# Kernel tuning notes

Measured on AMD Instinct MI355X. Metric: run time of the kernel, lower is better.

## Reference

```python
import jax, jax.numpy as jnp
import numpy as np

HEADS = 16
DIM_HEAD = 64
DIM = 1024
INNER = HEADS * DIM_HEAD  # 1024
DIM_OUT = 1024


def setup_inputs() -> dict:
    key = jax.random.key(0)
    k1, k2, k3, k4 = jax.random.split(key, 4)
    B, N = 4, 2048
    x = jax.random.normal(k1, (B, N, DIM), dtype=jnp.float32)
    # hk.Linear(inner_dim*3, with_bias=False): weight shape [in, out]
    w_qkv = jax.random.normal(k2, (DIM, INNER * 3), dtype=jnp.float32) / np.sqrt(DIM)
    # hk.Linear(dim_out): weight [INNER, DIM_OUT] + bias
    w_out = jax.random.normal(k3, (INNER, DIM_OUT), dtype=jnp.float32) / np.sqrt(INNER)
    b_out = jax.random.normal(k4, (DIM_OUT,), dtype=jnp.float32) * 0.01
    return {"x": x, "w_qkv": w_qkv, "w_out": w_out, "b_out": b_out}


def reference(x, w_qkv, w_out, b_out):
    B, N, _ = x.shape
    scale = DIM_HEAD ** -0.5
    qkv = x @ w_qkv  # [B, N, 3*INNER]
    q, k, v = jnp.split(qkv, 3, axis=-1)
    # b n (h d) -> b h n d
    split_heads = lambda t: t.reshape(B, N, HEADS, DIM_HEAD).transpose(0, 2, 1, 3)
    q, k, v = split_heads(q), split_heads(k), split_heads(v)
    dots = jnp.einsum('bhid,bhjd->bhij', q, k) * scale  # [B, H, N, N]
    attn = jax.nn.softmax(dots, axis=-1)
    out = jnp.einsum('bhij,bhjd->bhid', attn, v)  # [B, H, N, D]
    out = out.transpose(0, 2, 1, 3).reshape(B, N, INNER)  # b h n d -> b n (h d)
    return out @ w_out + b_out
```

## Files before the change

kernel.cpp:

```cpp
#include <hip/hip_runtime.h>
#include <cstdint>


typedef unsigned short ushort_t;
typedef _Float16 half_t;
typedef half_t half8 __attribute__((ext_vector_type(8)));
typedef half_t half4 __attribute__((ext_vector_type(4)));
typedef __fp16 fp16x2 __attribute__((ext_vector_type(2)));
typedef float floatx4 __attribute__((ext_vector_type(4)));
typedef ushort_t ushort8 __attribute__((ext_vector_type(8)));

#define QSCALE 0.18033688011112043f

__device__ __forceinline__ float bf2f(ushort_t h) {
  union { unsigned int u; float f; } v; v.u = ((unsigned int)h) << 16; return v.f;
}
__device__ __forceinline__ void async_copy16(const void* g, void* l) {
  __builtin_amdgcn_global_load_lds(
      reinterpret_cast<const __attribute__((address_space(1))) unsigned int*>(
          reinterpret_cast<uintptr_t>(g)),
      reinterpret_cast<__attribute__((address_space(3))) unsigned int*>(
          reinterpret_cast<uintptr_t>(l)),
      16, 0, 0);
}
__device__ __forceinline__ void lds_fence() {
  asm volatile("s_waitcnt lgkmcnt(0)" ::: "memory");
}
__device__ __forceinline__ void vm_fence() {
  asm volatile("s_waitcnt vmcnt(0)" ::: "memory");
}

__global__ __launch_bounds__(256) void prep_kernel(
    const void* __restrict__ x_raw, half_t* __restrict__ xb,
    const void* __restrict__ w_qkv_raw, half_t* __restrict__ WTqkv,
    const void* __restrict__ w_out_raw, half_t* __restrict__ WTout,
    const void* __restrict__ b_out_raw, float* __restrict__ bb) {
  __shared__ half_t tile[64][65];
  __shared__ int cnt;
  const int tid = threadIdx.x;
  if (tid == 0) cnt = 0;
  __syncthreads();
  {
    const ushort_t* xs = (const ushort_t*)x_raw;
    int local = 0;
    for (int i = tid; i < 8192; i += 256)
      if ((xs[i] & 0x7F80u) == 0x7F80u) ++local;
    if (local) atomicAdd(&cnt, local);
  }
  __syncthreads();
  const int isf32 = (cnt >= 2) ? 1 : 0;
  const int bid = blockIdx.x;

  if (bid < 4096) {
    const int i0 = (bid * 256 + tid) * 8;
    half8 o;
    if (isf32) {
      const floatx4* s = (const floatx4*)x_raw;
      const floatx4 a = s[(i0 >> 2)];
      const floatx4 b = s[(i0 >> 2) + 1];
#pragma unroll
      for (int j = 0; j < 4; ++j) { o[j] = (half_t)a[j]; o[4 + j] = (half_t)b[j]; }
    } else {
      const ushort8 u = *(const ushort8*)((const ushort_t*)x_raw + i0);
#pragma unroll
      for (int j = 0; j < 8; ++j) o[j] = (half_t)bf2f(u[j]);
    }
    *(half8*)&xb[i0] = o;
  } else if (bid < 5120) {
    const int t = bid - 4096;
    const int bx = t & 63;
    const int by = t >> 6;
    const void* src; half_t* dst; int C, c0;
    if (bx < 48) { src = w_qkv_raw; dst = WTqkv; C = 3072; c0 = bx * 64; }
    else         { src = w_out_raw; dst = WTout; C = 1024; c0 = (bx - 48) * 64; }
    const int R = 1024;
    const int r0 = by * 64;
    const int tx = tid & 63, ty = tid >> 6;
    if (isf32) {
      const float* s = (const float*)src;
      for (int i = ty; i < 64; i += 4) tile[i][tx] = (half_t)s[(size_t)(r0 + i) * C + (c0 + tx)];
    } else {
      const ushort_t* s = (const ushort_t*)src;
      for (int i = ty; i < 64; i += 4) tile[i][tx] = (half_t)bf2f(s[(size_t)(r0 + i) * C + (c0 + tx)]);
    }
    __syncthreads();
    for (int i = ty; i < 64; i += 4) dst[(size_t)(c0 + i) * R + (r0 + tx)] = tile[tx][i];
  } else {
#pragma unroll
    for (int j = 0; j < 4; ++j) {
      const int i = j * 256 + tid;
      bb[i] = isf32 ? ((const float*)b_out_raw)[i] : bf2f(((const ushort_t*)b_out_raw)[i]);
    }
  }
}

__global__ __launch_bounds__(512) void gemm_qkv_kernel(
    const half_t* __restrict__ X, const half_t* __restrict__ WT,
    half_t* __restrict__ Qb, half_t* __restrict__ Kb, half_t* __restrict__ VTb) {
  __shared__ half_t smem[65536];
  const int tid = threadIdx.x;
  const int wv = tid >> 6, lane = tid & 63;
  const int l15 = lane & 15, quad = lane >> 4, l7 = l15 & 7;
  const int wm = wv & 1, wn = wv >> 1;
  const int bid = blockIdx.x;
  const int xcd = bid & 7, idx = bid >> 3;
  const int mb = xcd * 4 + (idx & 3);
  const int nb = idx >> 2;
  const int rlo = lane >> 3, ci = lane & 7;
  const int sw_klo = (ci ^ rlo) * 8;
  const int rb0 = wv * 16, rb1 = wv * 16 + 8;

  const half_t* Ah[2] = {X + (size_t)(mb * 256) * 1024,
                         X + (size_t)(mb * 256 + 128) * 1024};
  const half_t* Bh[2] = {WT + (size_t)(nb * 256) * 1024,
                         WT + (size_t)(nb * 256 + 128) * 1024};

  floatx4 acc[8][4];
  const floatx4 z = {0.f, 0.f, 0.f, 0.f};
#pragma unroll
  for (int mi = 0; mi < 8; ++mi)
#pragma unroll
    for (int ni = 0; ni < 4; ++ni) acc[mi][ni] = z;

#pragma unroll
  for (int h = 0; h < 2; ++h) {
    async_copy16(Ah[h] + (size_t)(rb0 + rlo) * 1024 + sw_klo, &smem[h * 8192 + rb0 * 64]);
    async_copy16(Ah[h] + (size_t)(rb1 + rlo) * 1024 + sw_klo, &smem[h * 8192 + rb1 * 64]);
  }
#pragma unroll
  for (int h = 0; h < 2; ++h) {
    async_copy16(Bh[h] + (size_t)(rb0 + rlo) * 1024 + sw_klo, &smem[16384 + h * 8192 + rb0 * 64]);
    async_copy16(Bh[h] + (size_t)(rb1 + rlo) * 1024 + sw_klo, &smem[16384 + h * 8192 + rb1 * 64]);
  }

#pragma unroll 2
  for (int u = 0; u < 16; ++u) {
    const int b = u & 1, bn = b ^ 1;
    const int kn = ((u + 1) & 15) * 64;
    const int cb = b * 32768, cn = bn * 32768;

    async_copy16(Ah[0] + (size_t)(rb0 + rlo) * 1024 + kn + sw_klo, &smem[cn + rb0 * 64]);
    async_copy16(Ah[0] + (size_t)(rb1 + rlo) * 1024 + kn + sw_klo, &smem[cn + rb1 * 64]);
    asm volatile("s_waitcnt vmcnt(2)" ::: "memory");
    __builtin_amdgcn_s_barrier();
    __builtin_amdgcn_sched_barrier(0);

    half8 bf[4][2];
    const int bbase = cb + 16384 + (wn >> 1) * 8192 + ((wn & 1) * 64) * 64;
#pragma unroll
    for (int ni = 0; ni < 4; ++ni)
#pragma unroll
      for (int ks = 0; ks < 2; ++ks)
        bf[ni][ks] = *(const half8*)&smem[bbase + (ni * 16 + l15) * 64 + (((ks * 4 + quad) ^ l7) * 8)];
    const int abase = cb + wm * 8192;
    {
      half8 af[2][2];
#pragma unroll
      for (int m2 = 0; m2 < 2; ++m2)
#pragma unroll
        for (int ks = 0; ks < 2; ++ks)
          af[m2][ks] = *(const half8*)&smem[abase + ((0 * 2 + m2) * 16 + l15) * 64 + (((ks * 4 + quad) ^ l7) * 8)];
      __builtin_amdgcn_s_setprio(1);
#pragma unroll
      for (int ks = 0; ks < 2; ++ks)
#pragma unroll
        for (int m2 = 0; m2 < 2; ++m2)
#pragma unroll
          for (int ni = 0; ni < 4; ++ni)
            acc[0 * 2 + m2][ni] = __builtin_amdgcn_mfma_f32_16x16x32_f16(af[m2][ks], bf[ni][ks], acc[0 * 2 + m2][ni], 0, 0, 0);
      __builtin_amdgcn_s_setprio(0);
    }
    async_copy16(Ah[1] + (size_t)(rb0 + rlo) * 1024 + kn + sw_klo, &smem[cn + 8192 + rb0 * 64]);
    async_copy16(Ah[1] + (size_t)(rb1 + rlo) * 1024 + kn + sw_klo, &smem[cn + 8192 + rb1 * 64]);
    {
      half8 af[2][2];
#pragma unroll
      for (int m2 = 0; m2 < 2; ++m2)
#pragma unroll
        for (int ks = 0; ks < 2; ++ks)
          af[m2][ks] = *(const half8*)&smem[abase + ((1 * 2 + m2) * 16 + l15) * 64 + (((ks * 4 + quad) ^ l7) * 8)];
      __builtin_amdgcn_s_setprio(1);
#pragma unroll
      for (int ks = 0; ks < 2; ++ks)
#pragma unroll
        for (int m2 = 0; m2 < 2; ++m2)
#pragma unroll
          for (int ni = 0; ni < 4; ++ni)
            acc[1 * 2 + m2][ni] = __builtin_amdgcn_mfma_f32_16x16x32_f16(af[m2][ks], bf[ni][ks], acc[1 * 2 + m2][ni], 0, 0, 0);
      __builtin_amdgcn_s_setprio(0);
    }
    async_copy16(Bh[0] + (size_t)(rb0 + rlo) * 1024 + kn + sw_klo, &smem[cn + 16384 + rb0 * 64]);
    async_copy16(Bh[0] + (size_t)(rb1 + rlo) * 1024 + kn + sw_klo, &smem[cn + 16384 + rb1 * 64]);
    {
      half8 af[2][2];
#pragma unroll
      for (int m2 = 0; m2 < 2; ++m2)
#pragma unroll
        for (int ks = 0; ks < 2; ++ks)
          af[m2][ks] = *(const half8*)&smem[abase + ((2 * 2 + m2) * 16 + l15) * 64 + (((ks * 4 + quad) ^ l7) * 8)];
      __builtin_amdgcn_s_setprio(1);
#pragma unroll
      for (int ks = 0; ks < 2; ++ks)
#pragma unroll
        for (int m2 = 0; m2 < 2; ++m2)
#pragma unroll
          for (int ni = 0; ni < 4; ++ni)
            acc[2 * 2 + m2][ni] = __builtin_amdgcn_mfma_f32_16x16x32_f16(af[m2][ks], bf[ni][ks], acc[2 * 2 + m2][ni], 0, 0, 0);
      __builtin_amdgcn_s_setprio(0);
    }
    async_copy16(Bh[1] + (size_t)(rb0 + rlo) * 1024 + kn + sw_klo, &smem[cn + 24576 + rb0 * 64]);
    async_copy16(Bh[1] + (size_t)(rb1 + rlo) * 1024 + kn + sw_klo, &smem[cn + 24576 + rb1 * 64]);
    {
      half8 af[2][2];
#pragma unroll
      for (int m2 = 0; m2 < 2; ++m2)
#pragma unroll
        for (int ks = 0; ks < 2; ++ks)
          af[m2][ks] = *(const half8*)&smem[abase + ((3 * 2 + m2) * 16 + l15) * 64 + (((ks * 4 + quad) ^ l7) * 8)];
      __builtin_amdgcn_s_setprio(1);
#pragma unroll
      for (int ks = 0; ks < 2; ++ks)
#pragma unroll
        for (int m2 = 0; m2 < 2; ++m2)
#pragma unroll
          for (int ni = 0; ni < 4; ++ni)
            acc[3 * 2 + m2][ni] = __builtin_amdgcn_mfma_f32_16x16x32_f16(af[m2][ks], bf[ni][ks], acc[3 * 2 + m2][ni], 0, 0, 0);
      __builtin_amdgcn_s_setprio(0);
    }
  }

  vm_fence();
  __syncthreads();

  const int which = nb >> 2;
  if (which != 2) {
    const float sc = (which == 0) ? QSCALE : 1.0f;
#pragma unroll
    for (int mi = 0; mi < 8; ++mi)
#pragma unroll
      for (int ni = 0; ni < 4; ++ni) {
        const int col = wn * 64 + ni * 16 + l15;
        const int rowb = wm * 128 + mi * 16 + quad * 4;
#pragma unroll
        for (int r = 0; r < 4; ++r)
          smem[(rowb + r) * 256 + col] = (half_t)(acc[mi][ni][r] * sc);
      }
    __syncthreads();
    half_t* dstB = (which == 0) ? Qb : Kb;
    const int seg = tid & 31;
    const int hh = (nb & 3) * 4 + (seg >> 3);
    const int dd = (seg & 7) * 8;
#pragma unroll 4
    for (int i = 0; i < 16; ++i) {
      const int row = i * 16 + (tid >> 5);
      const half8 val = *(const half8*)&smem[row * 256 + seg * 8];
      const int rowg = mb * 256 + row;
      const int bb = rowg >> 11, nn = rowg & 2047;
      *(half8*)&dstB[(((size_t)(bb * 16 + hh)) * 2048 + nn) * 64 + dd] = val;
    }
  } else {
    const int nb2 = nb - 8;
    const int bb = mb >> 3;
    const int nn0 = (mb * 256) & 2047;
#pragma unroll
    for (int q = 0; q < 2; ++q) {
      if ((wn >> 1) == q) {
        const int dlb = (wn & 1) * 64;
#pragma unroll
        for (int mi = 0; mi < 8; ++mi)
#pragma unroll
          for (int ni = 0; ni < 4; ++ni) {
            const int dl = dlb + ni * 16 + l15;
            const int rowb = wm * 128 + mi * 16 + quad * 4;
#pragma unroll
            for (int r = 0; r < 4; ++r)
              smem[dl * 264 + rowb + r] = (half_t)acc[mi][ni][r];
          }
      }
      __syncthreads();
      const int npos = (tid & 127) * 2;
#pragma unroll 4
      for (int i = 0; i < 32; ++i) {
        const int dl = i * 4 + (tid >> 7);
        const int hh = nb2 * 4 + q * 2 + (dl >> 6);
        const int dd = dl & 63;
        const int koff = npos ^ ((dd & 8) ? 4 : 0);
        const uint32_t val = *(const uint32_t*)&smem[dl * 264 + npos];
        *(uint32_t*)&VTb[((size_t)((bb * 16 + hh) * 64 + dd)) * 2048 + nn0 + koff] = val;
      }
      __syncthreads();
    }
  }
}

__global__ __launch_bounds__(512) void attn_kernel(
    const half_t* __restrict__ Qb, const half_t* __restrict__ Kb,
    const half_t* __restrict__ VTb, half_t* __restrict__ Ob) {
  __shared__ half_t smem[16384];
  const int tid = threadIdx.x, wv = tid >> 6, lane = tid & 63;
  const int l15 = lane & 15, quad = lane >> 4;
  const int l7 = l15 & 7;
  const int bid = blockIdx.x;
  const int xcd = bid & 7, idx = bid >> 3;
  const int bh = ((idx & 7) << 3) + xcd;
  const int qt = idx >> 3;
  const int bq = bh >> 4, hh = bh & 15;
  const half_t* Qg = Qb + (size_t)bh * 2048 * 64;
  const half_t* Kg = Kb + (size_t)bh * 2048 * 64;
  const half_t* Vg = VTb + (size_t)bh * 64 * 2048;
  const int q0 = qt * 256;
  const int rlo = lane >> 3, ci = lane & 7;
  const int sw_klo = (ci ^ rlo) * 8;

  const int q1 = quad >> 1, qb0 = quad & 1, b3 = (l15 >> 3) & 1;
  int kx[2], vx[4];
#pragma unroll
  for (int ks = 0; ks < 2; ++ks) kx[ks] = ((ks * 4 + quad) ^ l7) * 8;
#pragma unroll
  for (int ki = 0; ki < 4; ++ki)
    vx[ki] = (((ki * 2 + q1) ^ l7) * 8) + ((qb0 ^ b3) * 4);

#pragma unroll
  for (int j = 0; j < 4; ++j) {
    const int rb = (wv * 4 + j) * 8;
    async_copy16(Qg + (size_t)(q0 + rb + rlo) * 64 + sw_klo, &smem[rb * 64]);
  }
  vm_fence();
  half8 aq[2][2];
#pragma unroll
  for (int ks = 0; ks < 2; ++ks)
#pragma unroll
    for (int qi = 0; qi < 2; ++qi) {
      const int rr = wv * 32 + qi * 16 + l15;
      aq[ks][qi] = *(const half8*)&smem[rr * 64 + (((ks * 4 + quad) ^ l7) * 8)];
    }
  __syncthreads();

  floatx4 o_acc[2][4];
  const floatx4 z = {0.f, 0.f, 0.f, 0.f};
  float l_st[2] = {0.f, 0.f};
#pragma unroll
  for (int qi = 0; qi < 2; ++qi)
#pragma unroll
    for (int di = 0; di < 4; ++di) o_acc[qi][di] = z;

  {
    const int rb = wv * 8;
    async_copy16(Kg + (size_t)(rb + rlo) * 64 + sw_klo, &smem[rb * 64]);
    async_copy16(Vg + (size_t)(rb + rlo) * 2048 + sw_klo, &smem[8192 + rb * 64]);
  }

#pragma unroll 2
  for (int t = 0; t < 32; ++t) {
    const int co = (t & 1) * 4096;
    const int po = 4096 - co;
    __syncthreads();
    if (t < 31) {
      const int rb = wv * 8;
      async_copy16(Kg + (size_t)((t + 1) * 64 + rb + rlo) * 64 + sw_klo,
                   &smem[po + rb * 64]);
      async_copy16(Vg + (size_t)(rb + rlo) * 2048 + (t + 1) * 64 + sw_klo,
                   &smem[8192 + po + rb * 64]);
    }
    const half_t* Kc = &smem[co];
    const half_t* Vc = &smem[8192 + co];

    floatx4 s_acc[4][2];
#pragma unroll
    for (int ki = 0; ki < 4; ++ki)
#pragma unroll
      for (int qi = 0; qi < 2; ++qi) s_acc[ki][qi] = z;
#pragma unroll
    for (int ks = 0; ks < 2; ++ks) {
      half8 bk[4];
#pragma unroll
      for (int ki = 0; ki < 4; ++ki)
        bk[ki] = *(const half8*)&Kc[(ki * 16 + l15) * 64 + kx[ks]];
      __builtin_amdgcn_s_setprio(1);
#pragma unroll
      for (int ki = 0; ki < 4; ++ki)
#pragma unroll
        for (int qi = 0; qi < 2; ++qi)
          s_acc[ki][qi] = __builtin_amdgcn_mfma_f32_16x16x32_f16(bk[ki], aq[ks][qi], s_acc[ki][qi], 0, 0, 0);
      __builtin_amdgcn_s_setprio(0);
    }

#pragma unroll
    for (int c = 0; c < 2; ++c) {
      half8 bv[4];
#pragma unroll
      for (int di = 0; di < 4; ++di) {
        union { half4 q[2]; half8 v; } b_;
        b_.q[0] = *(const half4*)&Vc[(di * 16 + l15) * 64 + vx[2 * c]];
        b_.q[1] = *(const half4*)&Vc[(di * 16 + l15) * 64 + vx[2 * c + 1]];
        bv[di] = b_.v;
      }
      union Ap { uint32_t u[4]; half8 h; } apu[2];
#pragma unroll
      for (int kii = 0; kii < 2; ++kii)
#pragma unroll
        for (int qi = 0; qi < 2; ++qi) {
          const int ki = c * 2 + kii;
          const float p0 = __builtin_amdgcn_exp2f(s_acc[ki][qi][0]);
          const float p1 = __builtin_amdgcn_exp2f(s_acc[ki][qi][1]);
          const float p2 = __builtin_amdgcn_exp2f(s_acc[ki][qi][2]);
          const float p3 = __builtin_amdgcn_exp2f(s_acc[ki][qi][3]);
          l_st[qi] += (p0 + p1) + (p2 + p3);
          union { fp16x2 v; uint32_t u; } lo_, hi_;
          lo_.v = __builtin_amdgcn_cvt_pkrtz(p0, p1);
          hi_.v = __builtin_amdgcn_cvt_pkrtz(p2, p3);
          apu[qi].u[kii * 2] = lo_.u;
          apu[qi].u[kii * 2 + 1] = hi_.u;
        }
      __builtin_amdgcn_s_setprio(1);
#pragma unroll
      for (int qi = 0; qi < 2; ++qi)
#pragma unroll
        for (int di = 0; di < 4; ++di)
          o_acc[qi][di] = __builtin_amdgcn_mfma_f32_16x16x32_f16(apu[qi].h, bv[di], o_acc[qi][di], 0, 0, 0);
      __builtin_amdgcn_s_setprio(0);
    }
  }

  float linv[2];
#pragma unroll
  for (int qi = 0; qi < 2; ++qi) {
    float rs = l_st[qi];
    rs += __shfl_xor(rs, 16);
    rs += __shfl_xor(rs, 32);
    linv[qi] = 1.0f / rs;
  }

  __syncthreads();
  const int c2 = (tid & 31) * 2;
  const int rbase = (tid >> 5) & 15;
#pragma unroll
  for (int p = 0; p < 2; ++p) {
    if ((wv >> 2) == p) {
      const int rw = (wv & 3) * 32;
#pragma unroll
      for (int qi = 0; qi < 2; ++qi)
#pragma unroll
        for (int r = 0; r < 4; ++r) {
          const float inv = __shfl(linv[qi], quad * 4 + r);
          const int rowl = rw + qi * 16 + quad * 4 + r;
#pragma unroll
          for (int di = 0; di < 4; ++di)
            smem[rowl * 72 + di * 16 + l15] = (half_t)(o_acc[qi][di][r] * inv);
        }
    }
    __syncthreads();
#pragma unroll 4
    for (int i = 0; i < 8; ++i) {
      const int rowl = i * 16 + rbase;
      const uint32_t val = *(const uint32_t*)&smem[rowl * 72 + c2];
      const int nn = q0 + p * 128 + rowl;
      *(uint32_t*)&Ob[((size_t)(bq * 2048 + nn)) * 1024 + hh * 64 + c2] = val;
    }
    __syncthreads();
  }
}

__global__ __launch_bounds__(256) void gemm_out_kernel(
    const half_t* __restrict__ A, const half_t* __restrict__ WT,
    const float* __restrict__ bias, float* __restrict__ out) {
  __shared__ half_t As[128 * 64];
  __shared__ half_t Bs[128 * 64];
  const int tid = threadIdx.x;
  const int wv = tid >> 6, lane = tid & 63;
  const int l15 = lane & 15, quad = lane >> 4;
  const int l7 = l15 & 7;
  const int wm = wv & 1, wn = wv >> 1;
  const int bid = blockIdx.x;
  const int xcd = bid & 7, idx = bid >> 3;
  const int mb = xcd * 8 + (idx & 7);
  const int nb = idx >> 3;
  const int rlo = lane >> 3, ci = lane & 7;
  const int sw_klo = (ci ^ rlo) * 8;

  floatx4 acc[4][4];
  const floatx4 z = {0.f, 0.f, 0.f, 0.f};
#pragma unroll
  for (int mi = 0; mi < 4; ++mi)
#pragma unroll
    for (int ni = 0; ni < 4; ++ni) acc[mi][ni] = z;

  const half_t* Abase = A + (size_t)mb * 128 * 1024;
  const half_t* Bbase = WT + (size_t)nb * 128 * 1024;

  for (int k0 = 0; k0 < 1024; k0 += 64) {
#pragma unroll
    for (int j = 0; j < 4; ++j) {
      const int rb = (wv * 4 + j) * 8;
      async_copy16(Abase + (size_t)(rb + rlo) * 1024 + k0 + sw_klo, &As[rb * 64]);
    }
#pragma unroll
    for (int j = 0; j < 4; ++j) {
      const int rb = (wv * 4 + j) * 8;
      async_copy16(Bbase + (size_t)(rb + rlo) * 1024 + k0 + sw_klo, &Bs[rb * 64]);
    }
    __syncthreads();
#pragma unroll
    for (int ks = 0; ks < 2; ++ks) {
      half8 af[4], bfv[4];
#pragma unroll
      for (int mi = 0; mi < 4; ++mi) {
        const int rr = wm * 64 + mi * 16 + l15;
        af[mi] = *(const half8*)&As[rr * 64 + (((ks * 4 + quad) ^ l7) * 8)];
      }
#pragma unroll
      for (int ni = 0; ni < 4; ++ni) {
        const int rr = wn * 64 + ni * 16 + l15;
        bfv[ni] = *(const half8*)&Bs[rr * 64 + (((ks * 4 + quad) ^ l7) * 8)];
      }
#pragma unroll
      for (int mi = 0; mi < 4; ++mi)
#pragma unroll
        for (int ni = 0; ni < 4; ++ni)
          acc[mi][ni] = __builtin_amdgcn_mfma_f32_16x16x32_f16(af[mi], bfv[ni], acc[mi][ni], 0, 0, 0);
    }
    __syncthreads();
  }

#pragma unroll
  for (int mi = 0; mi < 4; ++mi) {
#pragma unroll
    for (int ni = 0; ni < 4; ++ni) {
      const int colg = nb * 128 + wn * 64 + ni * 16 + l15;
      const float bs = bias[colg];
#pragma unroll
      for (int r = 0; r < 4; ++r) {
        const int rowg = mb * 128 + wm * 64 + mi * 16 + quad * 4 + r;
        out[(size_t)rowg * 1024 + colg] = acc[mi][ni][r] + bs;
      }
    }
  }
}

extern "C" void kernel_launch(void* const* d_in, const int* in_sizes, int n_in,
                              void* d_out, int out_size, void* d_ws, size_t ws_size,
                              hipStream_t stream) {
  const void* x_raw     = d_in[0];
  const void* w_qkv_raw = d_in[1];
  const void* w_out_raw = d_in[2];
  const void* b_out_raw = d_in[3];
  float* out = (float*)d_out;

  char* ws = (char*)d_ws;
  half_t* xb    = (half_t*)(ws);
  half_t* Qb    = (half_t*)(ws + ((size_t)16 << 20));
  half_t* Kb    = (half_t*)(ws + ((size_t)32 << 20));
  half_t* VTb   = (half_t*)(ws + ((size_t)48 << 20));
  half_t* WTqkv = (half_t*)(ws + ((size_t)64 << 20));
  half_t* WTout = (half_t*)(ws + ((size_t)70 << 20));
  float*  bb    = (float*)(ws + ((size_t)72 << 20));
  half_t* Ob    = xb;

  prep_kernel<<<5121, 256, 0, stream>>>(x_raw, xb, w_qkv_raw, WTqkv,
                                        w_out_raw, WTout, b_out_raw, bb);
  gemm_qkv_kernel<<<384, 512, 0, stream>>>(xb, WTqkv, Qb, Kb, VTb);
  attn_kernel<<<512, 512, 0, stream>>>(Qb, Kb, VTb, Ob);
  gemm_out_kernel<<<512, 256, 0, stream>>>(Ob, WTout, bb, out);
}
```

Before: 265.5 us.

## Double-buffer output GEMM with 128x256 tiles and interleaved async prefetch

Rewrites the output-projection GEMM to use 512-thread blocks computing 128x256 tiles, double-buffered LDS staging, and async global-to-LDS prefetch of the next K slice interleaved with MFMA groups. This is meant to hide global load latency that the old single-buffer loop exposed behind __syncthreads. It also adds a trailing barrier in the QKV GEMM loop. The larger tile halves the grid to 256 blocks, which can lower occupancy and load balance on the device.

```diff
diff --git a/kernel.cpp b/kernel.cpp
--- a/kernel.cpp
+++ b/kernel.cpp
@@ -227,6 +227,8 @@
             acc[3 * 2 + m2][ni] = __builtin_amdgcn_mfma_f32_16x16x32_f16(af[m2][ks], bf[ni][ks], acc[3 * 2 + m2][ni], 0, 0, 0);
       __builtin_amdgcn_s_setprio(0);
     }
+    __builtin_amdgcn_s_barrier();
+    __builtin_amdgcn_sched_barrier(0);
   }
 
   vm_fence();
@@ -461,15 +463,13 @@
   }
 }
 
-__global__ __launch_bounds__(256) void gemm_out_kernel(
+__global__ __launch_bounds__(512) void gemm_out_kernel(
     const half_t* __restrict__ A, const half_t* __restrict__ WT,
     const float* __restrict__ bias, float* __restrict__ out) {
-  __shared__ half_t As[128 * 64];
-  __shared__ half_t Bs[128 * 64];
+  __shared__ half_t smem[49152];
   const int tid = threadIdx.x;
   const int wv = tid >> 6, lane = tid & 63;
-  const int l15 = lane & 15, quad = lane >> 4;
-  const int l7 = l15 & 7;
+  const int l15 = lane & 15, quad = lane >> 4, l7 = l15 & 7;
   const int wm = wv & 1, wn = wv >> 1;
   const int bid = blockIdx.x;
   const int xcd = bid & 7, idx = bid >> 3;
@@ -477,6 +477,8 @@
   const int nb = idx >> 3;
   const int rlo = lane >> 3, ci = lane & 7;
   const int sw_klo = (ci ^ rlo) * 8;
+  const half_t* Abase = A + (size_t)(mb * 128) * 1024;
+  const half_t* Bbase = WT + (size_t)(nb * 256) * 1024;
 
   floatx4 acc[4][4];
   const floatx4 z = {0.f, 0.f, 0.f, 0.f};
@@ -485,48 +487,112 @@
 #pragma unroll
     for (int ni = 0; ni < 4; ++ni) acc[mi][ni] = z;
 
-  const half_t* Abase = A + (size_t)mb * 128 * 1024;
-  const half_t* Bbase = WT + (size_t)nb * 128 * 1024;
-
-  for (int k0 = 0; k0 < 1024; k0 += 64) {
-#pragma unroll
-    for (int j = 0; j < 4; ++j) {
-      const int rb = (wv * 4 + j) * 8;
-      async_copy16(Abase + (size_t)(rb + rlo) * 1024 + k0 + sw_klo, &As[rb * 64]);
-    }
-#pragma unroll
-    for (int j = 0; j < 4; ++j) {
-      const int rb = (wv * 4 + j) * 8;
-      async_copy16(Bbase + (size_t)(rb + rlo) * 1024 + k0 + sw_klo, &Bs[rb * 64]);
-    }
-    __syncthreads();
-#pragma unroll
-    for (int ks = 0; ks < 2; ++ks) {
-      half8 af[4], bfv[4];
-#pragma unroll
-      for (int mi = 0; mi < 4; ++mi) {
-        const int rr = wm * 64 + mi * 16 + l15;
-        af[mi] = *(const half8*)&As[rr * 64 + (((ks * 4 + quad) ^ l7) * 8)];
-      }
-#pragma unroll
-      for (int ni = 0; ni < 4; ++ni) {
-        const int rr = wn * 64 + ni * 16 + l15;
-        bfv[ni] = *(const half8*)&Bs[rr * 64 + (((ks * 4 + quad) ^ l7) * 8)];
-      }
-#pragma unroll
-      for (int mi = 0; mi < 4; ++mi)
+#pragma unroll
+  for (int j = 0; j < 2; ++j) {
+    const int ro = wv * 16 + j * 8;
+    async_copy16(Abase + (size_t)(ro + rlo) * 1024 + sw_klo, &smem[ro * 64]);
+  }
+#pragma unroll
+  for (int j = 0; j < 4; ++j) {
+    const int ro = wv * 32 + j * 8;
+    async_copy16(Bbase + (size_t)(ro + rlo) * 1024 + sw_klo, &smem[8192 + ro * 64]);
+  }
+
+#pragma unroll 2
+  for (int u = 0; u < 16; ++u) {
+    const int b = u & 1, bn = b ^ 1;
+    const int kn = ((u + 1) & 15) * 64;
+    const int cb = b * 24576, cn = bn * 24576;
+
+#pragma unroll
+    for (int j = 0; j < 2; ++j) {
+      const int ro = wv * 16 + j * 8;
+      async_copy16(Abase + (size_t)(ro + rlo) * 1024 + kn + sw_klo, &smem[cn + ro * 64]);
+    }
+    asm volatile("s_waitcnt vmcnt(2)" ::: "memory");
+    __builtin_amdgcn_s_barrier();
+    __builtin_amdgcn_sched_barrier(0);
+
+    half8 bf[4][2];
+    const int bbase2 = cb + 8192 + (wn * 64) * 64;
+#pragma unroll
+    for (int ni = 0; ni < 4; ++ni)
+#pragma unroll
+      for (int ks = 0; ks < 2; ++ks)
+        bf[ni][ks] = *(const half8*)&smem[bbase2 + (ni * 16 + l15) * 64 + (((ks * 4 + quad) ^ l7) * 8)];
+    const int abase = cb + (wm * 64) * 64;
+    {
+      half8 af[2];
+#pragma unroll
+      for (int ks = 0; ks < 2; ++ks)
+        af[ks] = *(const half8*)&smem[abase + (0 * 16 + l15) * 64 + (((ks * 4 + quad) ^ l7) * 8)];
+      __builtin_amdgcn_s_setprio(1);
+#pragma unroll
+      for (int ks = 0; ks < 2; ++ks)
 #pragma unroll
         for (int ni = 0; ni < 4; ++ni)
-          acc[mi][ni] = __builtin_amdgcn_mfma_f32_16x16x32_f16(af[mi], bfv[ni], acc[mi][ni], 0, 0, 0);
-    }
-    __syncthreads();
-  }
+          acc[0][ni] = __builtin_amdgcn_mfma_f32_16x16x32_f16(af[ks], bf[ni][ks], acc[0][ni], 0, 0, 0);
+      __builtin_amdgcn_s_setprio(0);
+    }
+#pragma unroll
+    for (int j = 0; j < 2; ++j) {
+      const int ro = wv * 32 + j * 8;
+      async_copy16(Bbase + (size_t)(ro + rlo) * 1024 + kn + sw_klo, &smem[cn + 8192 + ro * 64]);
+    }
+    {
+      half8 af[2];
+#pragma unroll
+      for (int ks = 0; ks < 2; ++ks)
+        af[ks] = *(const half8*)&smem[abase + (1 * 16 + l15) * 64 + (((ks * 4 + quad) ^ l7) * 8)];
+      __builtin_amdgcn_s_setprio(1);
+#pragma unroll
+      for (int ks = 0; ks < 2; ++ks)
+#pragma unroll
+        for (int ni = 0; ni < 4; ++ni)
+          acc[1][ni] = __builtin_amdgcn_mfma_f32_16x16x32_f16(af[ks], bf[ni][ks], acc[1][ni], 0, 0, 0);
+      __builtin_amdgcn_s_setprio(0);
+    }
+    {
+      const int ro = wv * 32 + 16;
+      async_copy16(Bbase + (size_t)(ro + rlo) * 1024 + kn + sw_klo, &smem[cn + 8192 + ro * 64]);
+      half8 af[2];
+#pragma unroll
+      for (int ks = 0; ks < 2; ++ks)
+        af[ks] = *(const half8*)&smem[abase + (2 * 16 + l15) * 64 + (((ks * 4 + quad) ^ l7) * 8)];
+      __builtin_amdgcn_s_setprio(1);
+#pragma unroll
+      for (int ks = 0; ks < 2; ++ks)
+#pragma unroll
+        for (int ni = 0; ni < 4; ++ni)
+          acc[2][ni] = __builtin_amdgcn_mfma_f32_16x16x32_f16(af[ks], bf[ni][ks], acc[2][ni], 0, 0, 0);
+      __builtin_amdgcn_s_setprio(0);
+    }
+    {
+      const int ro = wv * 32 + 24;
+      async_copy16(Bbase + (size_t)(ro + rlo) * 1024 + kn + sw_klo, &smem[cn + 8192 + ro * 64]);
+      half8 af[2];
+#pragma unroll
+      for (int ks = 0; ks < 2; ++ks)
+        af[ks] = *(const half8*)&smem[abase + (3 * 16 + l15) * 64 + (((ks * 4 + quad) ^ l7) * 8)];
+      __builtin_amdgcn_s_setprio(1);
+#pragma unroll
+      for (int ks = 0; ks < 2; ++ks)
+#pragma unroll
+        for (int ni = 0; ni < 4; ++ni)
+          acc[3][ni] = __builtin_amdgcn_mfma_f32_16x16x32_f16(af[ks], bf[ni][ks], acc[3][ni], 0, 0, 0);
+      __builtin_amdgcn_s_setprio(0);
+    }
+    __builtin_amdgcn_s_barrier();
+    __builtin_amdgcn_sched_barrier(0);
+  }
+
+  vm_fence();
 
 #pragma unroll
   for (int mi = 0; mi < 4; ++mi) {
 #pragma unroll
     for (int ni = 0; ni < 4; ++ni) {
-      const int colg = nb * 128 + wn * 64 + ni * 16 + l15;
+      const int colg = nb * 256 + wn * 64 + ni * 16 + l15;
       const float bs = bias[colg];
 #pragma unroll
       for (int r = 0; r < 4; ++r) {
@@ -560,5 +626,5 @@
                                         w_out_raw, WTout, b_out_raw, bb);
   gemm_qkv_kernel<<<384, 512, 0, stream>>>(xb, WTqkv, Qb, Kb, VTb);
   attn_kernel<<<512, 512, 0, stream>>>(Qb, Kb, VTb, Ob);
-  gemm_out_kernel<<<512, 256, 0, stream>>>(Ob, WTout, bb, out);
-}
+  gemm_out_kernel<<<256, 512, 0, stream>>>(Ob, WTout, bb, out);
+}
```

After: 260.0 us. -2.1%, faster.
